# Kernel optimization log

Measured on AMD Instinct MI355X. Metric: run time of the kernel, lower is better.

## Reference

```python
import jax, jax.numpy as jnp
import numpy as np

N_NODES = 100000
N_EDGES = 1600000
D_FEAT = 64
N_GRAPHS = 1000
D_MSG = 30


def _linear_init(key, fan_in, fan_out):
    kw, kb = jax.random.split(key)
    bound = 1.0 / np.sqrt(fan_in)
    W = jax.random.uniform(kw, (fan_in, fan_out), jnp.float32, -bound, bound)
    b = jax.random.uniform(kb, (fan_out,), jnp.float32, -bound, bound)
    return W, b


def setup_inputs() -> dict:
    key = jax.random.key(0)
    ks = jax.random.split(key, 8)
    edge_index = jax.random.randint(ks[0], (2, N_EDGES), 0, N_NODES, dtype=jnp.int64)
    node_attr = jax.random.normal(ks[1], (N_NODES, D_FEAT), jnp.float32)
    edge_attr = jax.random.normal(ks[2], (N_EDGES, D_FEAT), jnp.float32)
    batch = jnp.sort(jax.random.randint(ks[3], (N_NODES,), 0, N_GRAPHS, dtype=jnp.int64))
    W_msg, b_msg = _linear_init(ks[4], 3 * D_FEAT, D_MSG)   # MPL_1 edge MLP
    W1, b1 = _linear_init(ks[5], D_MSG, 20)
    W2, b2 = _linear_init(ks[6], 20, 10)
    W3, b3 = _linear_init(ks[7], 10, 1)
    return {
        "edge_index": edge_index, "node_attr": node_attr, "edge_attr": edge_attr,
        "batch": batch, "W_msg": W_msg, "b_msg": b_msg,
        "W1": W1, "b1": b1, "W2": W2, "b2": b2, "W3": W3, "b3": b3,
    }


def reference(edge_index, node_attr, edge_attr, batch,
              W_msg, b_msg, W1, b1, W2, b2, W3, b3):
    src, dst = edge_index[0], edge_index[1]
    # MPL_1: per-edge message = ReLU(Linear(concat(x_src, x_dst, e_attr))), sum-scatter to dst
    msg_in = jnp.concatenate([node_attr[src], node_attr[dst], edge_attr], axis=-1)  # [E, 3D]
    msg = jax.nn.relu(msg_in @ W_msg + b_msg)                                       # [E, 30]
    x = jax.ops.segment_sum(msg, dst, num_segments=N_NODES)                         # [N, 30]
    # per-node MLP head
    x = jax.nn.relu(x @ W1 + b1)                                                    # [N, 20]
    # graph-level pooling (segment_coo sum over batch index)
    x = jax.ops.segment_sum(x, batch, num_segments=N_GRAPHS)                        # [G, 20]
    x = jax.nn.relu(x @ W2 + b2)                                                    # [G, 10]
    return x @ W3 + b3                                                              # [G, 1]
```

## Files before the change

### kernel.cpp

```cpp
#include <hip/hip_runtime.h>

#define N_NODES    100000
#define N_EDGES    1600000
#define D_FEAT     64
#define N_GRAPHS   1000
#define D_MSG      30
#define D_H1       20
#define D_H2       10
#define P_STRIDE   64
#define N_SCAN     (N_NODES + 1)
#define N_SCAN_PAD 100004
#define NB_SCAN    ((N_SCAN + 1023) / 1024)

__global__ __launch_bounds__(256, 4) void node_proj_kernel(
    const float* __restrict__ node_attr,
    const float* __restrict__ W_msg,
    const float* __restrict__ b_msg,
    float*       __restrict__ P)
{
    __shared__ float wlds[128 * 32];
    const int t = threadIdx.x;
#pragma unroll
    for (int i = 0; i < 16; ++i) {
        const int f = t + i * 256;
        const int k = f >> 5, j = f & 31;
        wlds[f] = (j < D_MSG) ? W_msg[k * D_MSG + j] : 0.0f;
    }
    __syncthreads();

    const int n = blockIdx.x * 256 + t;
    if (n >= N_NODES) return;

    float a0[32], a1[32];
#pragma unroll
    for (int j = 0; j < 32; ++j) { a0[j] = 0.0f; a1[j] = 0.0f; }

    const float4* px = (const float4*)(node_attr + (size_t)n * D_FEAT);
#pragma unroll 4
    for (int q = 0; q < 16; ++q) {
        const float4 v = px[q];
        const float ev[4] = { v.x, v.y, v.z, v.w };
#pragma unroll
        for (int r = 0; r < 4; ++r) {
            const int k = 4 * q + r;
            const float4* w0 = (const float4*)&wlds[k * 32];
            const float4* w1 = (const float4*)&wlds[(64 + k) * 32];
#pragma unroll
            for (int jq = 0; jq < 8; ++jq) {
                const float4 w0v = w0[jq];
                const float4 w1v = w1[jq];
                a0[4*jq+0] = fmaf(ev[r], w0v.x, a0[4*jq+0]);
                a0[4*jq+1] = fmaf(ev[r], w0v.y, a0[4*jq+1]);
                a0[4*jq+2] = fmaf(ev[r], w0v.z, a0[4*jq+2]);
                a0[4*jq+3] = fmaf(ev[r], w0v.w, a0[4*jq+3]);
                a1[4*jq+0] = fmaf(ev[r], w1v.x, a1[4*jq+0]);
                a1[4*jq+1] = fmaf(ev[r], w1v.y, a1[4*jq+1]);
                a1[4*jq+2] = fmaf(ev[r], w1v.z, a1[4*jq+2]);
                a1[4*jq+3] = fmaf(ev[r], w1v.w, a1[4*jq+3]);
            }
        }
    }

    float4* pr = (float4*)(P + (size_t)n * P_STRIDE);
#pragma unroll
    for (int q = 0; q < 7; ++q)
        pr[q] = make_float4(a0[4*q] + b_msg[4*q], a0[4*q+1] + b_msg[4*q+1],
                            a0[4*q+2] + b_msg[4*q+2], a0[4*q+3] + b_msg[4*q+3]);
    pr[7] = make_float4(a0[28] + b_msg[28], a0[29] + b_msg[29], 0.0f, 0.0f);
#pragma unroll
    for (int q = 0; q < 7; ++q)
        pr[8 + q] = make_float4(a1[4*q], a1[4*q+1], a1[4*q+2], a1[4*q+3]);
    pr[15] = make_float4(a1[28], a1[29], 0.0f, 0.0f);
}

__global__ __launch_bounds__(256) void hist_kernel(
    const int* __restrict__ edge_index, int* __restrict__ cnt)
{
    const int e = blockIdx.x * 256 + threadIdx.x;
    atomicAdd(&cnt[edge_index[N_EDGES + e]], 1);
}

__global__ __launch_bounds__(1024) void scan_a(
    const int* __restrict__ cnt, int* __restrict__ offs, int* __restrict__ bsum)
{
    __shared__ int sh[1024];
    const int t = threadIdx.x;
    const int i = blockIdx.x * 1024 + t;
    const int v = (i < N_SCAN) ? cnt[i] : 0;
    sh[t] = v;
    __syncthreads();
#pragma unroll
    for (int off = 1; off < 1024; off <<= 1) {
        int u = 0;
        if (t >= off) u = sh[t - off];
        __syncthreads();
        if (t >= off) sh[t] += u;
        __syncthreads();
    }
    if (i < N_SCAN) offs[i] = sh[t] - v;
    if (t == 1023) bsum[blockIdx.x] = sh[1023];
}

__global__ __launch_bounds__(128) void scan_b(int* __restrict__ bsum)
{
    __shared__ int sh[128];
    const int t = threadIdx.x;
    const int v = (t < NB_SCAN) ? bsum[t] : 0;
    sh[t] = v;
    __syncthreads();
#pragma unroll
    for (int off = 1; off < 128; off <<= 1) {
        int u = 0;
        if (t >= off) u = sh[t - off];
        __syncthreads();
        if (t >= off) sh[t] += u;
        __syncthreads();
    }
    if (t < NB_SCAN) bsum[t] = sh[t] - v;
}

__global__ __launch_bounds__(1024) void scan_c(
    int* __restrict__ offs, const int* __restrict__ bsum, int* __restrict__ cur)
{
    const int i = blockIdx.x * 1024 + threadIdx.x;
    if (i < N_SCAN) {
        const int o = offs[i] + bsum[blockIdx.x];
        offs[i] = o;
        cur[i]  = o;
    }
}

__global__ __launch_bounds__(256) void scatter_rec(
    const int* __restrict__ edge_index, int* __restrict__ cur,
    int2* __restrict__ rec)
{
    const int e = blockIdx.x * 256 + threadIdx.x;
    const int s = edge_index[e];
    const int d = edge_index[N_EDGES + e];
    const int p = atomicAdd(&cur[d], 1);
    rec[p] = make_int2(e, s);
}

__global__ __launch_bounds__(256, 4) void fused_edge_reduce_head(
    const int2*  __restrict__ rec,
    const int*   __restrict__ offs,
    const float* __restrict__ P,
    const float* __restrict__ edge_attr,
    const float* __restrict__ W_msg,
    const int*   __restrict__ batch,
    const float* __restrict__ W1,
    const float* __restrict__ b1,
    float*       __restrict__ g)
{
    __shared__ float wlds[64 * 32];
    const int t = threadIdx.x;
#pragma unroll
    for (int i = 0; i < 8; ++i) {
        const int f = t + i * 256;
        const int k = f >> 5, j = f & 31;
        wlds[f] = (j < D_MSG) ? W_msg[(2 * D_FEAT + k) * D_MSG + j] : 0.0f;
    }
    __syncthreads();

    const int lane = t & 63;
    const int l16  = lane & 15;
    const int grp  = lane >> 4;
    const int wid  = t >> 6;
    const int n    = blockIdx.x * 16 + wid * 4 + grp;

    const int o0 = offs[n], o1 = offs[n + 1];
    const float4* p1 = (const float4*)(P + (size_t)n * P_STRIDE + 32);

    float acc[30];
#pragma unroll
    for (int j = 0; j < 30; ++j) acc[j] = 0.0f;

    for (int o = o0 + l16; o < o1; o += 16) {
        const int2 r2 = rec[o];
        const int e = r2.x, s = r2.y;
        const float4* p0 = (const float4*)(P + (size_t)s * P_STRIDE);
        const float4* pe = (const float4*)(edge_attr + (size_t)e * D_FEAT);

        float m[32];
#pragma unroll
        for (int q = 0; q < 8; ++q) {
            const float4 u = p0[q];
            const float4 w = p1[q];
            m[4*q+0] = u.x + w.x; m[4*q+1] = u.y + w.y;
            m[4*q+2] = u.z + w.z; m[4*q+3] = u.w + w.w;
        }
#pragma unroll 4
        for (int q = 0; q < 16; ++q) {
            const float4 v = pe[q];
            const float ev[4] = { v.x, v.y, v.z, v.w };
#pragma unroll
            for (int r = 0; r < 4; ++r) {
                const float4* wr = (const float4*)&wlds[(4 * q + r) * 32];
#pragma unroll
                for (int jq = 0; jq < 8; ++jq) {
                    const float4 wv = wr[jq];
                    m[4*jq+0] = fmaf(ev[r], wv.x, m[4*jq+0]);
                    m[4*jq+1] = fmaf(ev[r], wv.y, m[4*jq+1]);
                    m[4*jq+2] = fmaf(ev[r], wv.z, m[4*jq+2]);
                    m[4*jq+3] = fmaf(ev[r], wv.w, m[4*jq+3]);
                }
            }
        }
#pragma unroll
        for (int j = 0; j < 30; ++j) acc[j] += fmaxf(m[j], 0.0f);
    }

#pragma unroll
    for (int off = 1; off < 16; off <<= 1) {
#pragma unroll
        for (int j = 0; j < 30; ++j)
            acc[j] += __shfl_xor(acc[j], off, 16);
    }

    const int gi = batch[n];
    {
        float h = b1[l16];
#pragma unroll
        for (int j = 0; j < 30; ++j) h = fmaf(acc[j], W1[j * D_H1 + l16], h);
        h = fmaxf(h, 0.0f);
        if (h > 0.0f) atomicAdd(&g[(size_t)gi * D_H1 + l16], h);
    }
    if (l16 < 4) {
        const int t2 = 16 + l16;
        float h = b1[t2];
#pragma unroll
        for (int j = 0; j < 30; ++j) h = fmaf(acc[j], W1[j * D_H1 + t2], h);
        h = fmaxf(h, 0.0f);
        if (h > 0.0f) atomicAdd(&g[(size_t)gi * D_H1 + t2], h);
    }
}

__global__ __launch_bounds__(256) void graph_head_kernel(
    const float* __restrict__ g, const float* __restrict__ W2,
    const float* __restrict__ b2, const float* __restrict__ W3,
    const float* __restrict__ b3, float* __restrict__ out)
{
    const int i = blockIdx.x * 256 + threadIdx.x;
    if (i >= N_GRAPHS) return;

    float gv[D_H1];
    const float2* pg = (const float2*)(g + (size_t)i * D_H1);
#pragma unroll
    for (int j = 0; j < D_H1 / 2; ++j) {
        const float2 v = pg[j];
        gv[2*j] = v.x; gv[2*j+1] = v.y;
    }

    float h[D_H2];
#pragma unroll
    for (int tt = 0; tt < D_H2; ++tt) h[tt] = b2[tt];
#pragma unroll
    for (int j = 0; j < D_H1; ++j) {
#pragma unroll
        for (int tt = 0; tt < D_H2; ++tt) h[tt] = fmaf(gv[j], W2[j * D_H2 + tt], h[tt]);
    }

    float o = b3[0];
#pragma unroll
    for (int tt = 0; tt < D_H2; ++tt) o = fmaf(fmaxf(h[tt], 0.0f), W3[tt], o);

    out[i] = o;
}

extern "C" void kernel_launch(void* const* d_in, const int* in_sizes, int n_in,
                              void* d_out, int out_size, void* d_ws, size_t ws_size,
                              hipStream_t stream)
{
    (void)in_sizes; (void)n_in; (void)out_size; (void)ws_size;

    const int*   edge_index = (const int*)  d_in[0];
    const float* node_attr  = (const float*)d_in[1];
    const float* edge_attr  = (const float*)d_in[2];
    const int*   batch      = (const int*)  d_in[3];
    const float* W_msg      = (const float*)d_in[4];
    const float* b_msg      = (const float*)d_in[5];
    const float* W1         = (const float*)d_in[6];
    const float* b1         = (const float*)d_in[7];
    const float* W2         = (const float*)d_in[8];
    const float* b2         = (const float*)d_in[9];
    const float* W3         = (const float*)d_in[10];
    const float* b3         = (const float*)d_in[11];

    float* P    = (float*)d_ws;
    float* g    = P + (size_t)N_NODES * P_STRIDE;
    int*   cnt  = (int*)(g + (size_t)N_GRAPHS * D_H1);
    int*   offs = cnt + N_SCAN_PAD;
    int*   cur  = offs + N_SCAN_PAD;
    int*   bsum = cur + N_SCAN_PAD;
    int2*  rec  = (int2*)(bsum + 128);

    hipMemsetAsync(g, 0, ((size_t)N_GRAPHS * D_H1 + N_SCAN_PAD) * 4, stream);

    node_proj_kernel<<<(N_NODES + 255) / 256, 256, 0, stream>>>(
        node_attr, W_msg, b_msg, P);

    hist_kernel<<<N_EDGES / 256, 256, 0, stream>>>(edge_index, cnt);
    scan_a<<<NB_SCAN, 1024, 0, stream>>>(cnt, offs, bsum);
    scan_b<<<1, 128, 0, stream>>>(bsum);
    scan_c<<<NB_SCAN, 1024, 0, stream>>>(offs, bsum, cur);

    scatter_rec<<<N_EDGES / 256, 256, 0, stream>>>(edge_index, cur, rec);

    fused_edge_reduce_head<<<N_NODES / 16, 256, 0, stream>>>(
        rec, offs, P, edge_attr, W_msg, batch, W1, b1, g);

    graph_head_kernel<<<(N_GRAPHS + 255) / 256, 256, 0, stream>>>(
        g, W2, b2, W3, b3, (float*)d_out);
}
```

Before: 532.8 us.

## Fuse histogram into node projection; use 8 lanes per node with prefetched edge records

The edge-degree histogram is merged into the node projection kernel, so one launch covers both and the extra node blocks overlap with atomic counting. The main edge-reduce kernel now gives each node 8 lanes instead of 16, handles 32 nodes per block, raises the occupancy hint to 8 blocks per CU, and prefetches the next edge record one iteration ahead. The first layer of the MLP head is split into three column groups to match the 8-lane layout. Risks: nodes with many edges get fewer lanes each, and the occupancy hint of 8 may push the compiler to spill registers.

```diff
diff --git a/kernel.cpp b/kernel.cpp
--- a/kernel.cpp
+++ b/kernel.cpp
@@ -11,15 +11,28 @@
 #define N_SCAN     (N_NODES + 1)
 #define N_SCAN_PAD 100004
 #define NB_SCAN    ((N_SCAN + 1023) / 1024)
-
-__global__ __launch_bounds__(256, 4) void node_proj_kernel(
+#define NB_EDGE    (N_EDGES / 256)
+#define NB_NODE    ((N_NODES + 255) / 256)
+
+__global__ __launch_bounds__(256, 4) void node_proj_hist_kernel(
+    const int*   __restrict__ edge_index,
     const float* __restrict__ node_attr,
     const float* __restrict__ W_msg,
     const float* __restrict__ b_msg,
-    float*       __restrict__ P)
-{
+    float*       __restrict__ P,
+    int*         __restrict__ cnt)
+{
+    const int t   = threadIdx.x;
+    const int bid = blockIdx.x;
+
+    {
+        const int e = bid * 256 + t;
+        atomicAdd(&cnt[edge_index[N_EDGES + e]], 1);
+    }
+
+    if (bid >= NB_NODE) return;
+
     __shared__ float wlds[128 * 32];
-    const int t = threadIdx.x;
 #pragma unroll
     for (int i = 0; i < 16; ++i) {
         const int f = t + i * 256;
@@ -28,7 +41,7 @@
     }
     __syncthreads();
 
-    const int n = blockIdx.x * 256 + t;
+    const int n = bid * 256 + t;
     if (n >= N_NODES) return;
 
     float a0[32], a1[32];
@@ -73,13 +86,6 @@
     pr[15] = make_float4(a1[28], a1[29], 0.0f, 0.0f);
 }
 
-__global__ __launch_bounds__(256) void hist_kernel(
-    const int* __restrict__ edge_index, int* __restrict__ cnt)
-{
-    const int e = blockIdx.x * 256 + threadIdx.x;
-    atomicAdd(&cnt[edge_index[N_EDGES + e]], 1);
-}
-
 __global__ __launch_bounds__(1024) void scan_a(
     const int* __restrict__ cnt, int* __restrict__ offs, int* __restrict__ bsum)
 {
@@ -141,7 +147,7 @@
     rec[p] = make_int2(e, s);
 }
 
-__global__ __launch_bounds__(256, 4) void fused_edge_reduce_head(
+__global__ __launch_bounds__(256, 8) void fused_edge_reduce_head(
     const int2*  __restrict__ rec,
     const int*   __restrict__ offs,
     const float* __restrict__ P,
@@ -163,10 +169,10 @@
     __syncthreads();
 
     const int lane = t & 63;
-    const int l16  = lane & 15;
-    const int grp  = lane >> 4;
+    const int l8   = lane & 7;
+    const int grp  = lane >> 3;
     const int wid  = t >> 6;
-    const int n    = blockIdx.x * 16 + wid * 4 + grp;
+    const int n    = blockIdx.x * 32 + wid * 8 + grp;
 
     const int o0 = offs[n], o1 = offs[n + 1];
     const float4* p1 = (const float4*)(P + (size_t)n * P_STRIDE + 32);
@@ -175,9 +181,13 @@
 #pragma unroll
     for (int j = 0; j < 30; ++j) acc[j] = 0.0f;
 
-    for (int o = o0 + l16; o < o1; o += 16) {
-        const int2 r2 = rec[o];
-        const int e = r2.x, s = r2.y;
+    int  o = o0 + l8;
+    int2 r = (o < o1) ? rec[o] : make_int2(0, 0);
+    while (o < o1) {
+        const int e = r.x, s = r.y;
+        const int on = o + 8;
+        if (on < o1) r = rec[on];
+
         const float4* p0 = (const float4*)(P + (size_t)s * P_STRIDE);
         const float4* pe = (const float4*)(edge_attr + (size_t)e * D_FEAT);
 
@@ -194,44 +204,53 @@
             const float4 v = pe[q];
             const float ev[4] = { v.x, v.y, v.z, v.w };
 #pragma unroll
-            for (int r = 0; r < 4; ++r) {
-                const float4* wr = (const float4*)&wlds[(4 * q + r) * 32];
+            for (int rr = 0; rr < 4; ++rr) {
+                const float4* wr = (const float4*)&wlds[(4 * q + rr) * 32];
 #pragma unroll
                 for (int jq = 0; jq < 8; ++jq) {
                     const float4 wv = wr[jq];
-                    m[4*jq+0] = fmaf(ev[r], wv.x, m[4*jq+0]);
-                    m[4*jq+1] = fmaf(ev[r], wv.y, m[4*jq+1]);
-                    m[4*jq+2] = fmaf(ev[r], wv.z, m[4*jq+2]);
-                    m[4*jq+3] = fmaf(ev[r], wv.w, m[4*jq+3]);
+                    m[4*jq+0] = fmaf(ev[rr], wv.x, m[4*jq+0]);
+                    m[4*jq+1] = fmaf(ev[rr], wv.y, m[4*jq+1]);
+                    m[4*jq+2] = fmaf(ev[rr], wv.z, m[4*jq+2]);
+                    m[4*jq+3] = fmaf(ev[rr], wv.w, m[4*jq+3]);
                 }
             }
         }
 #pragma unroll
         for (int j = 0; j < 30; ++j) acc[j] += fmaxf(m[j], 0.0f);
-    }
-
-#pragma unroll
-    for (int off = 1; off < 16; off <<= 1) {
+        o = on;
+    }
+
+#pragma unroll
+    for (int off = 1; off < 8; off <<= 1) {
 #pragma unroll
         for (int j = 0; j < 30; ++j)
-            acc[j] += __shfl_xor(acc[j], off, 16);
+            acc[j] += __shfl_xor(acc[j], off, 8);
     }
 
     const int gi = batch[n];
     {
-        float h = b1[l16];
-#pragma unroll
-        for (int j = 0; j < 30; ++j) h = fmaf(acc[j], W1[j * D_H1 + l16], h);
+        float h = b1[l8];
+#pragma unroll
+        for (int j = 0; j < 30; ++j) h = fmaf(acc[j], W1[j * D_H1 + l8], h);
         h = fmaxf(h, 0.0f);
-        if (h > 0.0f) atomicAdd(&g[(size_t)gi * D_H1 + l16], h);
-    }
-    if (l16 < 4) {
-        const int t2 = 16 + l16;
-        float h = b1[t2];
-#pragma unroll
-        for (int j = 0; j < 30; ++j) h = fmaf(acc[j], W1[j * D_H1 + t2], h);
+        if (h > 0.0f) atomicAdd(&g[(size_t)gi * D_H1 + l8], h);
+    }
+    {
+        const int c = 8 + l8;
+        float h = b1[c];
+#pragma unroll
+        for (int j = 0; j < 30; ++j) h = fmaf(acc[j], W1[j * D_H1 + c], h);
         h = fmaxf(h, 0.0f);
-        if (h > 0.0f) atomicAdd(&g[(size_t)gi * D_H1 + t2], h);
+        if (h > 0.0f) atomicAdd(&g[(size_t)gi * D_H1 + c], h);
+    }
+    if (l8 < 4) {
+        const int c = 16 + l8;
+        float h = b1[c];
+#pragma unroll
+        for (int j = 0; j < 30; ++j) h = fmaf(acc[j], W1[j * D_H1 + c], h);
+        h = fmaxf(h, 0.0f);
+        if (h > 0.0f) atomicAdd(&g[(size_t)gi * D_H1 + c], h);
     }
 }
 
@@ -296,17 +315,16 @@
 
     hipMemsetAsync(g, 0, ((size_t)N_GRAPHS * D_H1 + N_SCAN_PAD) * 4, stream);
 
-    node_proj_kernel<<<(N_NODES + 255) / 256, 256, 0, stream>>>(
-        node_attr, W_msg, b_msg, P);
-
-    hist_kernel<<<N_EDGES / 256, 256, 0, stream>>>(edge_index, cnt);
+    node_proj_hist_kernel<<<NB_EDGE, 256, 0, stream>>>(
+        edge_index, node_attr, W_msg, b_msg, P, cnt);
+
     scan_a<<<NB_SCAN, 1024, 0, stream>>>(cnt, offs, bsum);
     scan_b<<<1, 128, 0, stream>>>(bsum);
     scan_c<<<NB_SCAN, 1024, 0, stream>>>(offs, bsum, cur);
 
-    scatter_rec<<<N_EDGES / 256, 256, 0, stream>>>(edge_index, cur, rec);
-
-    fused_edge_reduce_head<<<N_NODES / 16, 256, 0, stream>>>(
+    scatter_rec<<<NB_EDGE, 256, 0, stream>>>(edge_index, cur, rec);
+
+    fused_edge_reduce_head<<<N_NODES / 32, 256, 0, stream>>>(
         rec, offs, P, edge_attr, W_msg, batch, W1, b1, g);
 
     graph_head_kernel<<<(N_GRAPHS + 255) / 256, 256, 0, stream>>>(
```

Measured after the change: 625.6 us. 1.17x slower.
